# Optimization experiments

Measured on AMD Instinct MI355X. Metric: run time of the kernel, lower is better.

The kernel has to match this reference:

```python
import jax, jax.numpy as jnp
import numpy as np

N = 524288   # nodes (~1024x512 pixel graph)
C = 64       # channels
E = 8 * N    # 8-neighborhood edges
POOL = 4     # kernel_size**2 cluster downsample factor


def setup_inputs() -> dict:
    key = jax.random.key(0)
    k1, k2, k3 = jax.random.split(key, 3)
    x = jax.random.normal(k1, (N, C), dtype=jnp.float32)
    edge_index = jax.random.randint(k2, (2, E), 0, N, dtype=jnp.int32)
    # selection label per edge: 0 = self, 1..8 = compass directions
    selections = jax.random.randint(k3, (E,), 0, 9, dtype=jnp.int32)
    # each kernel_size^2 block of nodes maps to one coarse node
    cluster = (jnp.arange(N, dtype=jnp.int32) // POOL).astype(jnp.int32)
    return {"x": x, "edge_index": edge_index, "selections": selections,
            "cluster": cluster, "kernel_size": 2}


def reference(x, edge_index, selections, cluster, kernel_size):
    # maxPoolKernel: gather neighbor features along edges whose selection
    # direction lies inside the kernel_size x kernel_size pooling window,
    # segment-max them onto destination nodes (combined with the node's own
    # feature), then reduce nodes into coarse clusters with a segment-max.
    n_nodes = x.shape[0]
    n_clusters = n_nodes // POOL
    src, dst = edge_index[0], edge_index[1]
    neg = jnp.finfo(x.dtype).min
    in_window = (selections < kernel_size * kernel_size)[:, None]  # [E,1]
    msgs = jnp.where(in_window, x[src], neg)                        # [E,C]
    node_max = jnp.maximum(
        x, jax.ops.segment_max(msgs, dst, num_segments=n_nodes))    # [N,C]
    pooled = jax.ops.segment_max(node_max, cluster,
                                 num_segments=n_clusters)           # [M,C]
    return pooled
```

## Files before the change

### kernel.cpp

```cpp
#include <hip/hip_runtime.h>


#define NEG_FLT_MAX (-3.402823466e38f)
#define OFL_CAP 65536
#define SBC 512
#define SBC_BITS 9
#define SRC_BITS 23
#define STCAP 56
#define K1_WGS 256

typedef float fvec4 __attribute__((ext_vector_type(4)));
typedef int   ivec4 __attribute__((ext_vector_type(4)));

__device__ __forceinline__ float4 fmax4(float4 a, float4 b) {
    return make_float4(fmaxf(a.x, b.x), fmaxf(a.y, b.y),
                       fmaxf(a.z, b.z), fmaxf(a.w, b.w));
}

__device__ __forceinline__ void ofl_push(unsigned* __restrict__ ofl,
                                         unsigned m, unsigned src) {
    unsigned idx = atomicAdd(&ofl[0], 1u);
    if (idx < OFL_CAP) { ofl[1 + 2 * idx] = m; ofl[2 + 2 * idx] = src; }
}


__global__ __launch_bounds__(256) void partition_kernel(
        const int* __restrict__ edge_index,
        const int* __restrict__ selections,
        const int* __restrict__ ksz,
        unsigned* __restrict__ sb_count,
        unsigned* __restrict__ pairs,
        unsigned* __restrict__ ofl,
        int E, int shift, int sbn, int scap) {
    __shared__ unsigned scnt[256];
    __shared__ unsigned stage[256 * STCAP];

    for (int i = threadIdx.x; i < sbn; i += 256) scnt[i] = 0;
    __syncthreads();

    int ks = ksz[0];
    int ks2 = ks * ks;

    long long per_wg = ((long long)E + K1_WGS - 1) / K1_WGS;
    per_wg = (per_wg + 2047) & ~2047LL;
    long long base = (long long)blockIdx.x * per_wg;
    long long wend = base + per_wg;
    if (wend > E) wend = E;

    for (long long t = base; t < wend; t += 2048) {
        long long e0 = t + (long long)threadIdx.x * 8;
        int sel[8], dst[8], src[8];
        if (((E & 3) == 0) && (e0 + 8 <= (long long)E)) {
            ivec4 s0 = __builtin_nontemporal_load((const ivec4*)&selections[e0]);
            ivec4 s1 = __builtin_nontemporal_load((const ivec4*)&selections[e0 + 4]);
            ivec4 d0 = __builtin_nontemporal_load((const ivec4*)&edge_index[E + e0]);
            ivec4 d1 = __builtin_nontemporal_load((const ivec4*)&edge_index[E + e0 + 4]);
            ivec4 r0 = __builtin_nontemporal_load((const ivec4*)&edge_index[e0]);
            ivec4 r1 = __builtin_nontemporal_load((const ivec4*)&edge_index[e0 + 4]);
            #pragma unroll
            for (int i = 0; i < 4; ++i) {
                sel[i] = s0[i]; sel[4 + i] = s1[i];
                dst[i] = d0[i]; dst[4 + i] = d1[i];
                src[i] = r0[i]; src[4 + i] = r1[i];
            }
        } else {
            #pragma unroll
            for (int i = 0; i < 8; ++i) {
                long long e = e0 + i;
                sel[i] = (e < E) ? selections[e] : ks2;
                dst[i] = (e < E) ? edge_index[E + e] : 0;
                src[i] = (e < E) ? edge_index[e] : 0;
            }
        }

        #pragma unroll
        for (int i = 0; i < 8; ++i) {
            if (sel[i] >= ks2) continue;
            unsigned m  = ((unsigned)dst[i]) >> shift;
            unsigned sb = m >> SBC_BITS;
            unsigned packed = ((m & (SBC - 1)) << SRC_BITS) | (unsigned)src[i];
            unsigned pos = atomicAdd(&scnt[sb], 1u);
            if (pos < STCAP) {
                stage[sb * STCAP + pos] = packed;
            } else {
                unsigned g = atomicAdd(&sb_count[sb], 1u);
                if (g < (unsigned)scap) pairs[(size_t)sb * scap + g] = packed;
                else ofl_push(ofl, m, (unsigned)src[i]);
            }
        }
    }
    __syncthreads();

    if ((int)threadIdx.x < sbn) {
        int sb = threadIdx.x;
        unsigned c = scnt[sb];
        if (c > STCAP) c = STCAP;
        if (c) {
            unsigned g = atomicAdd(&sb_count[sb], c);
            for (unsigned i = 0; i < c; ++i) {
                unsigned gi = g + i;
                unsigned p = stage[sb * STCAP + i];
                if (gi < (unsigned)scap) {
                    pairs[(size_t)sb * scap + gi] = p;
                } else {
                    ofl_push(ofl, ((unsigned)sb << SBC_BITS) | (p >> SRC_BITS),
                             p & ((1u << SRC_BITS) - 1));
                }
            }
        }
    }
}


__global__ __launch_bounds__(256) void binsort_kernel(
        const unsigned* __restrict__ sb_count,
        const unsigned* __restrict__ pairs,
        unsigned* __restrict__ counts,
        unsigned* __restrict__ records,
        unsigned* __restrict__ ofl,
        int M, int scap, int cap) {
    __shared__ unsigned lcnt[SBC];
    int sb = blockIdx.x;
    for (int i = threadIdx.x; i < SBC; i += 256) lcnt[i] = 0;
    __syncthreads();

    int nb = (int)sb_count[sb];
    if (nb > scap) nb = scap;
    unsigned mbase = (unsigned)sb << SBC_BITS;

    for (int i = threadIdx.x; i < nb; i += 256) {
        unsigned p    = pairs[(size_t)sb * scap + i];
        unsigned ml   = p >> SRC_BITS;
        unsigned srcv = p & ((1u << SRC_BITS) - 1);
        unsigned pos  = atomicAdd(&lcnt[ml], 1u);
        unsigned m    = mbase + ml;
        if (pos < (unsigned)cap) {
            records[(size_t)m * cap + pos] = srcv;
        } else {
            ofl_push(ofl, m, srcv);
        }
    }
    __syncthreads();

    for (int i = threadIdx.x; i < SBC; i += 256) {
        unsigned m = mbase + i;
        if ((int)m < M) counts[m] = lcnt[i];
    }
}


__global__ __launch_bounds__(256) void gather_kernel(
        const float* __restrict__ x,
        const unsigned* __restrict__ records,
        const unsigned* __restrict__ counts,
        const unsigned* __restrict__ ofl,
        float* __restrict__ out, int M, int pool, int cap) {
    int lane = threadIdx.x & 63;
    int wave = threadIdx.x >> 6;
    int m = blockIdx.x * 4 + wave;
    if (m >= M) return;
    int r  = lane >> 4;
    int c4 = lane & 15;
    const float4* x4 = (const float4*)x;
    unsigned mbase = (unsigned)(m * pool);

    unsigned cnt_raw = counts[m];
    int cnt_c = min((int)cnt_raw, cap);
    unsigned rec = mbase;
    if (lane < cnt_c)
        rec = records[(size_t)m * cap + lane];

    float4 acc = make_float4(NEG_FLT_MAX, NEG_FLT_MAX, NEG_FLT_MAX, NEG_FLT_MAX);

    for (int k = r; k < pool; k += 4)
        acc = fmax4(acc, x4[((size_t)mbase + k) * 16 + c4]);

    for (int base = 0; base < cnt_c; base += 16) {
        unsigned s0 = (unsigned)__shfl((int)rec, base + r,      64);
        unsigned s1 = (unsigned)__shfl((int)rec, base + 4 + r,  64);
        unsigned s2 = (unsigned)__shfl((int)rec, base + 8 + r,  64);
        unsigned s3 = (unsigned)__shfl((int)rec, base + 12 + r, 64);
        float4 v0 = x4[(size_t)s0 * 16 + c4];
        float4 v1 = x4[(size_t)s1 * 16 + c4];
        float4 v2 = x4[(size_t)s2 * 16 + c4];
        float4 v3 = x4[(size_t)s3 * 16 + c4];
        acc = fmax4(acc, fmax4(fmax4(v0, v1), fmax4(v2, v3)));
    }

    unsigned n = ofl[0];
    if (n > 0) {
        if (n > OFL_CAP) n = OFL_CAP;
        for (unsigned i = 0; i < n; ++i) {
            unsigned mi = ofl[1 + 2 * i];
            if (mi == (unsigned)m) {
                unsigned si = ofl[2 + 2 * i];
                acc = fmax4(acc, x4[(size_t)si * 16 + c4]);
            }
        }
    }

    for (int off = 16; off < 64; off <<= 1) {
        acc.x = fmaxf(acc.x, __shfl_xor(acc.x, off, 64));
        acc.y = fmaxf(acc.y, __shfl_xor(acc.y, off, 64));
        acc.z = fmaxf(acc.z, __shfl_xor(acc.z, off, 64));
        acc.w = fmaxf(acc.w, __shfl_xor(acc.w, off, 64));
    }
    if (r == 0) {
        fvec4 o = { acc.x, acc.y, acc.z, acc.w };
        __builtin_nontemporal_store(o, (fvec4*)&((float4*)out)[(size_t)m * 16 + c4]);
    }
}


__device__ __forceinline__ unsigned enc_f(float f) {
    unsigned b = __float_as_uint(f);
    return (b & 0x80000000u) ? ~b : (b | 0x80000000u);
}
__device__ __forceinline__ float dec_f(unsigned u) {
    unsigned b = (u & 0x80000000u) ? (u & 0x7fffffffu) : ~u;
    return __uint_as_float(b);
}

__global__ void pool_init_kernel(const float* __restrict__ x,
                                 unsigned* __restrict__ out_u, int M, int pool) {
    int idx = blockIdx.x * blockDim.x + threadIdx.x;
    if (idx >= M * 16) return;
    int m = idx >> 4, c4 = idx & 15;
    const float4* x4 = (const float4*)x;
    size_t base = (size_t)m * pool;
    float4 v = x4[base * 16 + c4];
    for (int k = 1; k < pool; ++k) v = fmax4(v, x4[(base + k) * 16 + c4]);
    uint4 u; u.x = enc_f(v.x); u.y = enc_f(v.y); u.z = enc_f(v.z); u.w = enc_f(v.w);
    ((uint4*)out_u)[idx] = u;
}

__global__ void edge_scatter_kernel(const float* __restrict__ x,
                                    const int* __restrict__ edge_index,
                                    const int* __restrict__ selections,
                                    const int* __restrict__ cluster,
                                    const int* __restrict__ ksz,
                                    unsigned* __restrict__ out_u, int E) {
    int t = blockIdx.x * blockDim.x + threadIdx.x;
    int e = t >> 4;
    if (e >= E) return;
    int c4 = t & 15;
    int ks = ksz[0];
    if (selections[e] >= ks * ks) return;
    int src = edge_index[e];
    int m = cluster[edge_index[E + e]];
    float4 v = ((const float4*)x)[(size_t)src * 16 + c4];
    unsigned e0 = enc_f(v.x), e1 = enc_f(v.y), e2 = enc_f(v.z), e3 = enc_f(v.w);
    unsigned* o = out_u + (size_t)m * 64 + c4 * 4;
    uint4 cur = *(const uint4*)o;
    if (e0 > cur.x) atomicMax(o + 0, e0);
    if (e1 > cur.y) atomicMax(o + 1, e1);
    if (e2 > cur.z) atomicMax(o + 2, e2);
    if (e3 > cur.w) atomicMax(o + 3, e3);
}

__global__ void decode_kernel(unsigned* __restrict__ out_u, int total4) {
    int idx = blockIdx.x * blockDim.x + threadIdx.x;
    if (idx >= total4) return;
    uint4 u = ((uint4*)out_u)[idx];
    float4 f; f.x = dec_f(u.x); f.y = dec_f(u.y); f.z = dec_f(u.z); f.w = dec_f(u.w);
    ((float4*)out_u)[idx] = f;
}


extern "C" void kernel_launch(void* const* d_in, const int* in_sizes, int n_in,
                              void* d_out, int out_size, void* d_ws, size_t ws_size,
                              hipStream_t stream) {
    const float* x          = (const float*)d_in[0];
    const int*   edge_index = (const int*)d_in[1];
    const int*   selections = (const int*)d_in[2];
    const int*   cluster    = (const int*)d_in[3];
    const int*   ksz        = (const int*)d_in[4];

    const int C = 64;
    int N = in_sizes[0] / C;
    int E = in_sizes[1] / 2;
    int M = out_size / C;
    int pool = N / M;

    int shift = -1;
    if (pool > 0 && (pool & (pool - 1)) == 0) {
        shift = 0;
        while ((1 << shift) < pool) ++shift;
    }

    int sbn = (M % SBC == 0) ? (M / SBC) : 0;
    bool planS = (shift >= 0) && sbn >= 1 && sbn <= 256 &&
                 N <= (1 << SRC_BITS) && E > 0 && M > 0;

    const int cap = 32;
    size_t off_sb = 0, off_ofl = 0, off_counts = 0, off_records = 0, off_pairs = 0;
    int scap = 0;
    if (planS) {
        const int scap_try[3] = {12288, 8192, 6144};
        bool fits = false;
        for (int a = 0; a < 3 && !fits; ++a) {
            int sc = scap_try[a];
            off_sb      = 0;
            off_ofl     = (size_t)sbn;
            off_counts  = (off_ofl + 1 + 2 * (size_t)OFL_CAP + 15) & ~(size_t)15;
            off_records = off_counts + (size_t)M;
            off_pairs   = off_records + (size_t)M * cap;
            size_t need = (off_pairs + (size_t)sbn * sc) * 4;
            if (ws_size >= need) { scap = sc; fits = true; }
        }
        if (!fits) planS = false;
    }

    if (planS) {
        unsigned* ws       = (unsigned*)d_ws;
        unsigned* sb_count = ws + off_sb;
        unsigned* ofl      = ws + off_ofl;
        unsigned* counts   = ws + off_counts;
        unsigned* records  = ws + off_records;
        unsigned* pairs    = ws + off_pairs;
        float*    out      = (float*)d_out;

        hipMemsetAsync(sb_count, 0, ((size_t)sbn + 1) * 4, stream);

        partition_kernel<<<K1_WGS, 256, 0, stream>>>(
            edge_index, selections, ksz, sb_count, pairs, ofl,
            E, shift, sbn, scap);
        binsort_kernel<<<sbn, 256, 0, stream>>>(
            sb_count, pairs, counts, records, ofl, M, scap, cap);
        gather_kernel<<<(M + 3) / 4, 256, 0, stream>>>(
            x, records, counts, ofl, out, M, pool, cap);
    } else {
        unsigned* out_u = (unsigned*)d_out;
        int t1 = M * 16;
        pool_init_kernel<<<(t1 + 255) / 256, 256, 0, stream>>>(x, out_u, M, pool);
        long long t2 = (long long)E * 16;
        edge_scatter_kernel<<<(int)((t2 + 255) / 256), 256, 0, stream>>>(
            x, edge_index, selections, cluster, ksz, out_u, E);
        decode_kernel<<<(t1 + 255) / 256, 256, 0, stream>>>(out_u, t1);
    }
}
```

Before: 334.3 us.

## Stage bin lists in LDS, widen binsort/partition, unroll gather to fixed 32 records

Binsort now builds each cluster's source list in shared memory and writes it out with coalesced uint4 stores instead of scattered per-record global writes, using 1024-thread blocks. Partition uses more workgroups with a smaller staging buffer. The gather kernel drops its variable-trip loop and always issues 32 loads (8 per row group), padding unused slots with the cluster's own node. This cuts scattered stores and loop overhead but adds 64KB of LDS per block and redundant loads when counts are small.

After: 315.6 us. 5.6% less time.

```diff
diff --git a/kernel.cpp b/kernel.cpp
--- a/kernel.cpp
+++ b/kernel.cpp
@@ -6,8 +6,9 @@
 #define SBC 512
 #define SBC_BITS 9
 #define SRC_BITS 23
-#define STCAP 56
-#define K1_WGS 256
+#define STCAP 16
+#define K1_WGS 1024
+#define RCAP 32
 
 typedef float fvec4 __attribute__((ext_vector_type(4)));
 typedef int   ivec4 __attribute__((ext_vector_type(4)));
@@ -112,37 +113,38 @@
 }
 
 
-__global__ __launch_bounds__(256) void binsort_kernel(
+__global__ __launch_bounds__(1024) void binsort_kernel(
         const unsigned* __restrict__ sb_count,
         const unsigned* __restrict__ pairs,
         unsigned* __restrict__ counts,
         unsigned* __restrict__ records,
         unsigned* __restrict__ ofl,
-        int M, int scap, int cap) {
+        int M, int scap) {
     __shared__ unsigned lcnt[SBC];
+    __shared__ unsigned lists[SBC * RCAP];
     int sb = blockIdx.x;
-    for (int i = threadIdx.x; i < SBC; i += 256) lcnt[i] = 0;
+    for (int i = threadIdx.x; i < SBC; i += 1024) lcnt[i] = 0;
     __syncthreads();
 
     int nb = (int)sb_count[sb];
     if (nb > scap) nb = scap;
     unsigned mbase = (unsigned)sb << SBC_BITS;
 
-    for (int i = threadIdx.x; i < nb; i += 256) {
+    for (int i = threadIdx.x; i < nb; i += 1024) {
         unsigned p    = pairs[(size_t)sb * scap + i];
         unsigned ml   = p >> SRC_BITS;
         unsigned srcv = p & ((1u << SRC_BITS) - 1);
         unsigned pos  = atomicAdd(&lcnt[ml], 1u);
-        unsigned m    = mbase + ml;
-        if (pos < (unsigned)cap) {
-            records[(size_t)m * cap + pos] = srcv;
-        } else {
-            ofl_push(ofl, m, srcv);
-        }
+        if (pos < (unsigned)RCAP) lists[ml * RCAP + pos] = srcv;
+        else ofl_push(ofl, mbase + ml, srcv);
     }
     __syncthreads();
 
-    for (int i = threadIdx.x; i < SBC; i += 256) {
+    uint4* dst4 = (uint4*)(records + (size_t)mbase * RCAP);
+    const uint4* src4 = (const uint4*)lists;
+    for (int i = threadIdx.x; i < (SBC * RCAP) / 4; i += 1024)
+        dst4[i] = src4[i];
+    for (int i = threadIdx.x; i < SBC; i += 1024) {
         unsigned m = mbase + i;
         if ((int)m < M) counts[m] = lcnt[i];
     }
@@ -154,7 +156,7 @@
         const unsigned* __restrict__ records,
         const unsigned* __restrict__ counts,
         const unsigned* __restrict__ ofl,
-        float* __restrict__ out, int M, int pool, int cap) {
+        float* __restrict__ out, int M, int pool) {
     int lane = threadIdx.x & 63;
     int wave = threadIdx.x >> 6;
     int m = blockIdx.x * 4 + wave;
@@ -165,27 +167,32 @@
     unsigned mbase = (unsigned)(m * pool);
 
     unsigned cnt_raw = counts[m];
-    int cnt_c = min((int)cnt_raw, cap);
-    unsigned rec = mbase;
-    if (lane < cnt_c)
-        rec = records[(size_t)m * cap + lane];
-
+    unsigned rr = records[(size_t)m * RCAP + (lane & (RCAP - 1))];
     float4 acc = make_float4(NEG_FLT_MAX, NEG_FLT_MAX, NEG_FLT_MAX, NEG_FLT_MAX);
-
     for (int k = r; k < pool; k += 4)
         acc = fmax4(acc, x4[((size_t)mbase + k) * 16 + c4]);
 
-    for (int base = 0; base < cnt_c; base += 16) {
-        unsigned s0 = (unsigned)__shfl((int)rec, base + r,      64);
-        unsigned s1 = (unsigned)__shfl((int)rec, base + 4 + r,  64);
-        unsigned s2 = (unsigned)__shfl((int)rec, base + 8 + r,  64);
-        unsigned s3 = (unsigned)__shfl((int)rec, base + 12 + r, 64);
-        float4 v0 = x4[(size_t)s0 * 16 + c4];
-        float4 v1 = x4[(size_t)s1 * 16 + c4];
-        float4 v2 = x4[(size_t)s2 * 16 + c4];
-        float4 v3 = x4[(size_t)s3 * 16 + c4];
-        acc = fmax4(acc, fmax4(fmax4(v0, v1), fmax4(v2, v3)));
-    }
+    int cnt_c = min((int)cnt_raw, RCAP);
+    unsigned rec = (lane < cnt_c) ? rr : mbase;
+
+    unsigned s0 = (unsigned)__shfl((int)rec,  0 + r, 64);
+    unsigned s1 = (unsigned)__shfl((int)rec,  4 + r, 64);
+    unsigned s2 = (unsigned)__shfl((int)rec,  8 + r, 64);
+    unsigned s3 = (unsigned)__shfl((int)rec, 12 + r, 64);
+    unsigned s4 = (unsigned)__shfl((int)rec, 16 + r, 64);
+    unsigned s5 = (unsigned)__shfl((int)rec, 20 + r, 64);
+    unsigned s6 = (unsigned)__shfl((int)rec, 24 + r, 64);
+    unsigned s7 = (unsigned)__shfl((int)rec, 28 + r, 64);
+    float4 v0 = x4[(size_t)s0 * 16 + c4];
+    float4 v1 = x4[(size_t)s1 * 16 + c4];
+    float4 v2 = x4[(size_t)s2 * 16 + c4];
+    float4 v3 = x4[(size_t)s3 * 16 + c4];
+    float4 v4 = x4[(size_t)s4 * 16 + c4];
+    float4 v5 = x4[(size_t)s5 * 16 + c4];
+    float4 v6 = x4[(size_t)s6 * 16 + c4];
+    float4 v7 = x4[(size_t)s7 * 16 + c4];
+    acc = fmax4(acc, fmax4(fmax4(fmax4(v0, v1), fmax4(v2, v3)),
+                           fmax4(fmax4(v4, v5), fmax4(v6, v7))));
 
     unsigned n = ofl[0];
     if (n > 0) {
@@ -292,7 +299,6 @@
     bool planS = (shift >= 0) && sbn >= 1 && sbn <= 256 &&
                  N <= (1 << SRC_BITS) && E > 0 && M > 0;
 
-    const int cap = 32;
     size_t off_sb = 0, off_ofl = 0, off_counts = 0, off_records = 0, off_pairs = 0;
     int scap = 0;
     if (planS) {
@@ -304,7 +310,7 @@
             off_ofl     = (size_t)sbn;
             off_counts  = (off_ofl + 1 + 2 * (size_t)OFL_CAP + 15) & ~(size_t)15;
             off_records = off_counts + (size_t)M;
-            off_pairs   = off_records + (size_t)M * cap;
+            off_pairs   = off_records + (size_t)M * RCAP;
             size_t need = (off_pairs + (size_t)sbn * sc) * 4;
             if (ws_size >= need) { scap = sc; fits = true; }
         }
@@ -325,10 +331,10 @@
         partition_kernel<<<K1_WGS, 256, 0, stream>>>(
             edge_index, selections, ksz, sb_count, pairs, ofl,
             E, shift, sbn, scap);
-        binsort_kernel<<<sbn, 256, 0, stream>>>(
-            sb_count, pairs, counts, records, ofl, M, scap, cap);
+        binsort_kernel<<<sbn, 1024, 0, stream>>>(
+            sb_count, pairs, counts, records, ofl, M, scap);
         gather_kernel<<<(M + 3) / 4, 256, 0, stream>>>(
-            x, records, counts, ofl, out, M, pool, cap);
+            x, records, counts, ofl, out, M, pool);
     } else {
         unsigned* out_u = (unsigned*)d_out;
         int t1 = M * 16;
```
